# Kernel optimization log

Measured on AMD Instinct MI355X. Metric: run time of the kernel, lower is better.

Reference implementation:

```python
import jax, jax.numpy as jnp
import numpy as np

EPS = 1e-7  # tf.keras.backend.epsilon()
NUM_ROUTING = 3


def squash(v, axis=-1):
    s2 = jnp.sum(jnp.square(v), axis=axis, keepdims=True)
    scale = s2 / (1.0 + s2)
    return scale * v / jnp.sqrt(s2 + EPS)


def setup_inputs() -> dict:
    key = jax.random.key(0)
    kx, kw = jax.random.split(key)
    B, IN_CAPS, IN_DIM = 64, 2048, 16
    NUM_CAPS, OUT_DIM = 32, 16  # OUT_DIM must equal IN_DIM per the tf.matmul in call()
    x = jax.random.normal(kx, (B, IN_CAPS, IN_DIM), dtype=jnp.float32)
    # glorot_uniform over [in_caps, num_caps, in_dim, out_dim]
    limit = float(np.sqrt(6.0 / (IN_DIM + OUT_DIM)))
    W = jax.random.uniform(kw, (IN_CAPS, NUM_CAPS, IN_DIM, OUT_DIM),
                           minval=-limit, maxval=limit, dtype=jnp.float32)
    return {"x": x, "W": W}


def reference(x, W):
    # u_hat[b,i,j,d] = sum_k W[i,j,d,k] * x[b,i,k]   (tf.matmul(W, x[...,None]))
    u_hat = jnp.einsum('ijdk,bik->bijd', W, x)  # [B, in_caps, num_caps, dim]
    b = jnp.zeros(u_hat.shape[:-1], dtype=u_hat.dtype)  # [B, in_caps, num_caps]
    outputs = None
    for i in range(NUM_ROUTING):
        c = jax.nn.softmax(b, axis=2)                       # over num_caps
        s = jnp.einsum('bij,bijd->bjd', c, u_hat)           # weighted sum over in_caps
        outputs = squash(s)                                 # [B, num_caps, dim]
        if i < NUM_ROUTING - 1:
            b = b + jnp.einsum('bijd,bjd->bij', u_hat, outputs)  # agreement
    return outputs
```

## Files before the change

### kernel.cpp

```cpp
#include <hip/hip_runtime.h>
#include <cstdio>


#define IC    2048
#define NC    32
#define OD    16
#define JD    512
#define NIC   256
#define IPB   (IC/NIC)
#define EPS_SQ 1e-7f

typedef short  s16x4  __attribute__((ext_vector_type(4)));
typedef short  s16x8  __attribute__((ext_vector_type(8)));
typedef float  f32x16 __attribute__((ext_vector_type(16)));

__device__ inline short bfc(float f) {
  unsigned u = __builtin_bit_cast(unsigned, f);
  unsigned r = (u + 0x7FFFu + ((u >> 16) & 1u)) >> 16;
  return (short)(unsigned short)r;
}
__device__ inline float bf2f(short s) {
  return __builtin_bit_cast(float, ((unsigned)(unsigned short)s) << 16);
}
__device__ inline f32x16 fz16() {
  f32x16 z;
#pragma unroll
  for (int q = 0; q < 16; q++) z[q] = 0.f;
  return z;
}

__global__ __launch_bounds__(256) void k_prep_x(const float* __restrict__ x,
                                                unsigned short* __restrict__ xp) {
  int t = blockIdx.x * 256 + threadIdx.x;
  int l  = t & 63;
  int bg = (t >> 6) & 1;
  int i  = t >> 7;
  int b  = bg * 32 + (l & 31);
  int hi = l >> 5;
  const float* s = x + ((size_t)b * IC + i) * 16 + 4 * hi;
  float4 v0 = *(const float4*)(s);
  float4 v1 = *(const float4*)(s + 8);
  s16x8 r;
  r[0] = bfc(v0.x); r[1] = bfc(v0.y); r[2] = bfc(v0.z); r[3] = bfc(v0.w);
  r[4] = bfc(v1.x); r[5] = bfc(v1.y); r[6] = bfc(v1.z); r[7] = bfc(v1.w);
  *(s16x8*)(xp + (size_t)t * 8) = r;
}

__global__ __launch_bounds__(256) void k_prep_w(const float* __restrict__ W,
                                                unsigned short* __restrict__ wp) {
  __shared__ unsigned lds[512 * 9];
  const int i = blockIdx.x;
  const int t = threadIdx.x;
  const float* src = W + (size_t)i * 8192;
#pragma unroll
  for (int q = 0; q < 8; q++) {
    int idx = q * 256 + t;
    float4 v = *(const float4*)(src + (size_t)idx * 4);
    unsigned p0 = ((unsigned)(unsigned short)bfc(v.x)) |
                  (((unsigned)(unsigned short)bfc(v.y)) << 16);
    unsigned p1 = ((unsigned)(unsigned short)bfc(v.z)) |
                  (((unsigned)(unsigned short)bfc(v.w)) << 16);
    int jd = idx >> 2;
    int slot = (idx & 3) * 2;
    lds[jd * 9 + slot]     = p0;
    lds[jd * 9 + slot + 1] = p1;
  }
  __syncthreads();
#pragma unroll
  for (int q = 0; q < 4; q++) {
    int f = q * 256 + t;
    int mt = f >> 6, l = f & 63;
    int col = l & 31, hi = l >> 5;
    int jd = mt * 32 + col;
    unsigned r0 = lds[jd * 9 + 2 * hi];
    unsigned r1 = lds[jd * 9 + 2 * hi + 1];
    unsigned r2 = lds[jd * 9 + 2 * hi + 4];
    unsigned r3 = lds[jd * 9 + 2 * hi + 5];
    uint4 o; o.x = r0; o.y = r1; o.z = r2; o.w = r3;
    *(uint4*)(wp + ((size_t)i * 1024 + f) * 8) = o;
  }
}

template <bool FIRST, bool PACKED>
__global__ __launch_bounds__(256, 2) void k_pass(const float* __restrict__ W,
                                                 const unsigned short* __restrict__ Wp,
                                                 const unsigned short* __restrict__ xp,
                                                 const float* __restrict__ ST,
                                                 _Float16* __restrict__ part) {
  __shared__ float lg[32][33];
  const int bid = blockIdx.x;
  const int bg  = bid & 1;
  const int ic  = bid >> 1;
  const int tid = threadIdx.x;
  const int w   = tid >> 6;
  const int l   = tid & 63;
  const int col = l & 31;
  const int hi  = l >> 5;

  f32x16 sa[4];
#pragma unroll
  for (int m = 0; m < 4; m++) sa[m] = fz16();

  s16x8 svA[4], svB[4];
  if (!FIRST) {
#pragma unroll
    for (int m = 0; m < 4; m++) {
      int mt = w * 4 + m;
#pragma unroll
      for (int r = 0; r < 16; r++) {
        int row = (r & 3) + 8 * (r >> 2) + 4 * hi;
        float v = ST[(size_t)(mt * 32 + row) * 64 + bg * 32 + col];
        short h = bfc(v);
        if (r < 8) svA[m][r] = h; else svB[m][r - 8] = h;
      }
    }
  }

  for (int ii = 0; ii < IPB; ii++) {
    int i = ic * IPB + ii;
    s16x8 xv = *(const s16x8*)(xp + ((size_t)i * 2 + bg) * 512 + (size_t)l * 8);
    s16x4 xlo = __builtin_shufflevector(xv, xv, 0, 1, 2, 3);
    s16x4 xhi = __builtin_shufflevector(xv, xv, 4, 5, 6, 7);

    s16x4 wlo[4], whi[4];
    if (PACKED) {
#pragma unroll
      for (int m = 0; m < 4; m++) {
        s16x8 wv = *(const s16x8*)(Wp + ((size_t)i * 1024 + (w * 4 + m) * 64 + l) * 8);
        wlo[m] = __builtin_shufflevector(wv, wv, 0, 1, 2, 3);
        whi[m] = __builtin_shufflevector(wv, wv, 4, 5, 6, 7);
      }
    } else {
#pragma unroll
      for (int m = 0; m < 4; m++) {
        int jd = (w * 4 + m) * 32 + col;
        const float* wq = W + ((size_t)i * JD + jd) * 16 + 4 * hi;
        float4 a0 = *(const float4*)(wq);
        float4 a1 = *(const float4*)(wq + 8);
        s16x4 t0; t0[0]=bfc(a0.x); t0[1]=bfc(a0.y); t0[2]=bfc(a0.z); t0[3]=bfc(a0.w);
        s16x4 t1; t1[0]=bfc(a1.x); t1[1]=bfc(a1.y); t1[2]=bfc(a1.z); t1[3]=bfc(a1.w);
        wlo[m] = t0; whi[m] = t1;
      }
    }

    f32x16 D[4];
#pragma unroll
    for (int m = 0; m < 4; m++) {
      f32x16 acc = FIRST ? sa[m] : fz16();
      acc = __builtin_amdgcn_mfma_f32_32x32x8bf16_1k(wlo[m], xlo, acc, 0, 0, 0);
      acc = __builtin_amdgcn_mfma_f32_32x32x8bf16_1k(whi[m], xhi, acc, 0, 0, 0);
      if (FIRST) sa[m] = acc; else D[m] = acc;
    }

    if (!FIRST) {
#pragma unroll
      for (int m = 0; m < 4; m++) {
        float pe = 0.f, po = 0.f;
#pragma unroll
        for (int r = 0; r < 8; r++)  pe += D[m][r]     * bf2f(svA[m][r]);
#pragma unroll
        for (int r = 0; r < 8; r++)  po += D[m][r + 8] * bf2f(svB[m][r]);
        pe += __shfl_xor(pe, 32);
        po += __shfl_xor(po, 32);
        int mt = w * 4 + m;
        if (l < 32) { lg[2 * mt][col] = pe; lg[2 * mt + 1][col] = po; }
      }
      __syncthreads();
      {
        int bb = w * 8 + (l >> 3);
        int sub = l & 7;
        float v0 = lg[sub * 4 + 0][bb], v1 = lg[sub * 4 + 1][bb];
        float v2 = lg[sub * 4 + 2][bb], v3 = lg[sub * 4 + 3][bb];
        float mx = fmaxf(fmaxf(v0, v1), fmaxf(v2, v3));
        mx = fmaxf(mx, __shfl_xor(mx, 1));
        mx = fmaxf(mx, __shfl_xor(mx, 2));
        mx = fmaxf(mx, __shfl_xor(mx, 4));
        v0 = __expf(v0 - mx); v1 = __expf(v1 - mx);
        v2 = __expf(v2 - mx); v3 = __expf(v3 - mx);
        float sm = v0 + v1 + v2 + v3;
        sm += __shfl_xor(sm, 1);
        sm += __shfl_xor(sm, 2);
        sm += __shfl_xor(sm, 4);
        float iv = 1.0f / sm;
        lg[sub * 4 + 0][bb] = v0 * iv; lg[sub * 4 + 1][bb] = v1 * iv;
        lg[sub * 4 + 2][bb] = v2 * iv; lg[sub * 4 + 3][bb] = v3 * iv;
      }
      __syncthreads();
#pragma unroll
      for (int m = 0; m < 4; m++) {
        int mt = w * 4 + m;
        float ce = lg[2 * mt][col];
        float co = lg[2 * mt + 1][col];
#pragma unroll
        for (int r = 0; r < 8; r++)  sa[m][r]     += ce * D[m][r];
#pragma unroll
        for (int r = 0; r < 8; r++)  sa[m][r + 8] += co * D[m][r + 8];
      }
      __syncthreads();
    }
  }

  const float sc = FIRST ? (1.0f / 32.0f) : 1.0f;
#pragma unroll
  for (int m = 0; m < 4; m++) {
    int mt = w * 4 + m;
#pragma unroll
    for (int r = 0; r < 16; r++) {
      int row = (r & 3) + 8 * (r >> 2) + 4 * hi;
      int jd = mt * 32 + row;
      part[(((size_t)bg * JD + jd) * NIC + ic) * 32 + col] = (_Float16)(sa[m][r] * sc);
    }
  }
}

__global__ __launch_bounds__(512) void k_red(const _Float16* __restrict__ part,
                                             float* __restrict__ red) {
  int bid = blockIdx.x;
  int bg = bid & 1, j = (bid >> 1) & 31, q = bid >> 6;
  int t = threadIdx.x;
  int b = t & 31, d = t >> 5;
  int jd = j * 16 + d;
  const _Float16* p = part + (((size_t)(bg * JD + jd) * NIC) + q * 32) * 32 + b;
  float a0 = 0.f, a1 = 0.f, a2 = 0.f, a3 = 0.f;
#pragma unroll
  for (int qq = 0; qq < 32; qq += 4) {
    a0 += (float)p[(size_t)(qq + 0) * 32];
    a1 += (float)p[(size_t)(qq + 1) * 32];
    a2 += (float)p[(size_t)(qq + 2) * 32];
    a3 += (float)p[(size_t)(qq + 3) * 32];
  }
  red[((size_t)(bg * 32 + j) * 8 + q) * 512 + t] = (a0 + a1) + (a2 + a3);
}

template <bool FIRST, bool FINAL>
__global__ __launch_bounds__(512) void k_squash2(const float* __restrict__ red,
                                                 float* __restrict__ ST,
                                                 float* __restrict__ out) {
  __shared__ float sl[16][33];
  int bid = blockIdx.x;
  int bg = bid & 1, j = bid >> 1;
  int t = threadIdx.x;
  int b = t & 31, d = t >> 5;
  float s = 0.f;
#pragma unroll
  for (int q = 0; q < 8; q++) s += red[((size_t)(bg * 32 + j) * 8 + q) * 512 + t];
  sl[d][b] = s * s;
  __syncthreads();
  float s2 = 0.f;
#pragma unroll
  for (int dd = 0; dd < 16; dd++) s2 += sl[dd][b];
  float o = s * s2 / ((1.0f + s2) * sqrtf(s2 + EPS_SQ));
  int jd = j * 16 + d;
  if (FINAL) {
    out[((size_t)(bg * 32 + b) * NC + j) * OD + d] = o;
  } else if (FIRST) {
    ST[(size_t)jd * 64 + bg * 32 + b] = o;
  } else {
    ST[(size_t)jd * 64 + bg * 32 + b] += o;
  }
}

extern "C" void kernel_launch(void* const* d_in, const int* in_sizes, int n_in,
                              void* d_out, int out_size, void* d_ws, size_t ws_size,
                              hipStream_t stream) {
  (void)in_sizes; (void)n_in; (void)out_size;
  const float* x = (const float*)d_in[0];
  const float* W = (const float*)d_in[1];
  float* out = (float*)d_out;

  const size_t off_xp  = 0;
  const size_t off_st  = (size_t)4 << 20;
  const size_t off_red = off_st + ((size_t)256 << 10);
  const size_t off_pt  = off_red + ((size_t)1 << 20);
  const size_t off_wp  = off_pt + (size_t)2 * JD * NIC * 32 * sizeof(_Float16);
  const size_t need_base = off_wp + 1024;
  const size_t need_full = off_wp + (size_t)IC * 1024 * 16 + 1024;
  fprintf(stderr, "[caps] ws_size=%zu need_base=%zu need_full=%zu\n",
          ws_size, need_base, need_full);
  if (ws_size < need_base) return;
  const bool packed = (ws_size >= need_full);

  unsigned short* xp = (unsigned short*)((char*)d_ws + off_xp);
  float*          ST = (float*)((char*)d_ws + off_st);
  float*         red = (float*)((char*)d_ws + off_red);
  _Float16*     part = (_Float16*)((char*)d_ws + off_pt);
  unsigned short* Wp = (unsigned short*)((char*)d_ws + off_wp);

  k_prep_x<<<dim3(1024), dim3(256), 0, stream>>>(x, xp);
  if (packed) {
    k_prep_w<<<dim3(2048), dim3(256), 0, stream>>>(W, Wp);
    k_pass<true, true><<<dim3(512), dim3(256), 0, stream>>>(W, Wp, xp, ST, part);
  } else {
    k_pass<true, false><<<dim3(512), dim3(256), 0, stream>>>(W, Wp, xp, ST, part);
  }
  k_red<<<dim3(512), dim3(512), 0, stream>>>(part, red);
  k_squash2<true, false><<<dim3(64), dim3(512), 0, stream>>>(red, ST, out);

  for (int pass = 1; pass < 3; pass++) {
    if (packed) {
      k_pass<false, true><<<dim3(512), dim3(256), 0, stream>>>(W, Wp, xp, ST, part);
    } else {
      k_pass<false, false><<<dim3(512), dim3(256), 0, stream>>>(W, Wp, xp, ST, part);
    }
    k_red<<<dim3(512), dim3(512), 0, stream>>>(part, red);
    if (pass == 1) {
      k_squash2<false, false><<<dim3(64), dim3(512), 0, stream>>>(red, ST, out);
    } else {
      k_squash2<false, true><<<dim3(64), dim3(512), 0, stream>>>(red, ST, out);
    }
  }
}
```

Before: 190.2 us.

## Simplify routing softmax to one barrier, merge prep kernels, single-stage reduction

Merges the x and W bf16 prep kernels into one launch and drops the unpacked-W fallback path. In the routing pass, the softmax skips max subtraction and cross-wave LDS transposes. It keeps exp values in registers and reduces only the per-batch normaliser through a small double-buffered LDS array, leaving one barrier per input capsule instead of three. The two-stage partial reduction becomes a single k_red producing final sums, and ST is kept in fp32 rather than re-rounded to bf16. Dropping max subtraction risks overflow if the logits grow large.

```diff
diff --git a/kernel.cpp b/kernel.cpp
--- a/kernel.cpp
+++ b/kernel.cpp
@@ -19,9 +19,6 @@
   unsigned r = (u + 0x7FFFu + ((u >> 16) & 1u)) >> 16;
   return (short)(unsigned short)r;
 }
-__device__ inline float bf2f(short s) {
-  return __builtin_bit_cast(float, ((unsigned)(unsigned short)s) << 16);
-}
 __device__ inline f32x16 fz16() {
   f32x16 z;
 #pragma unroll
@@ -29,65 +26,70 @@
   return z;
 }
 
-__global__ __launch_bounds__(256) void k_prep_x(const float* __restrict__ x,
-                                                unsigned short* __restrict__ xp) {
-  int t = blockIdx.x * 256 + threadIdx.x;
-  int l  = t & 63;
-  int bg = (t >> 6) & 1;
-  int i  = t >> 7;
-  int b  = bg * 32 + (l & 31);
-  int hi = l >> 5;
-  const float* s = x + ((size_t)b * IC + i) * 16 + 4 * hi;
-  float4 v0 = *(const float4*)(s);
-  float4 v1 = *(const float4*)(s + 8);
-  s16x8 r;
-  r[0] = bfc(v0.x); r[1] = bfc(v0.y); r[2] = bfc(v0.z); r[3] = bfc(v0.w);
-  r[4] = bfc(v1.x); r[5] = bfc(v1.y); r[6] = bfc(v1.z); r[7] = bfc(v1.w);
-  *(s16x8*)(xp + (size_t)t * 8) = r;
-}
-
-__global__ __launch_bounds__(256) void k_prep_w(const float* __restrict__ W,
-                                                unsigned short* __restrict__ wp) {
+__global__ __launch_bounds__(256) void k_prep(const float* __restrict__ W,
+                                              const float* __restrict__ x,
+                                              unsigned short* __restrict__ wp,
+                                              unsigned short* __restrict__ xp) {
   __shared__ unsigned lds[512 * 9];
-  const int i = blockIdx.x;
+  const int bid = blockIdx.x;
   const int t = threadIdx.x;
-  const float* src = W + (size_t)i * 8192;
-#pragma unroll
-  for (int q = 0; q < 8; q++) {
-    int idx = q * 256 + t;
-    float4 v = *(const float4*)(src + (size_t)idx * 4);
-    unsigned p0 = ((unsigned)(unsigned short)bfc(v.x)) |
-                  (((unsigned)(unsigned short)bfc(v.y)) << 16);
-    unsigned p1 = ((unsigned)(unsigned short)bfc(v.z)) |
-                  (((unsigned)(unsigned short)bfc(v.w)) << 16);
-    int jd = idx >> 2;
-    int slot = (idx & 3) * 2;
-    lds[jd * 9 + slot]     = p0;
-    lds[jd * 9 + slot + 1] = p1;
-  }
-  __syncthreads();
-#pragma unroll
-  for (int q = 0; q < 4; q++) {
-    int f = q * 256 + t;
-    int mt = f >> 6, l = f & 63;
-    int col = l & 31, hi = l >> 5;
-    int jd = mt * 32 + col;
-    unsigned r0 = lds[jd * 9 + 2 * hi];
-    unsigned r1 = lds[jd * 9 + 2 * hi + 1];
-    unsigned r2 = lds[jd * 9 + 2 * hi + 4];
-    unsigned r3 = lds[jd * 9 + 2 * hi + 5];
-    uint4 o; o.x = r0; o.y = r1; o.z = r2; o.w = r3;
-    *(uint4*)(wp + ((size_t)i * 1024 + f) * 8) = o;
-  }
-}
-
-template <bool FIRST, bool PACKED>
-__global__ __launch_bounds__(256, 2) void k_pass(const float* __restrict__ W,
-                                                 const unsigned short* __restrict__ Wp,
+  if (bid < 2048) {
+    const int i = bid;
+    const float* src = W + (size_t)i * 8192;
+#pragma unroll
+    for (int q = 0; q < 8; q++) {
+      int idx = q * 256 + t;
+      float4 v = *(const float4*)(src + (size_t)idx * 4);
+      unsigned p0 = ((unsigned)(unsigned short)bfc(v.x)) |
+                    (((unsigned)(unsigned short)bfc(v.y)) << 16);
+      unsigned p1 = ((unsigned)(unsigned short)bfc(v.z)) |
+                    (((unsigned)(unsigned short)bfc(v.w)) << 16);
+      int jd = idx >> 2;
+      int slot = (idx & 3) * 2;
+      lds[jd * 9 + slot]     = p0;
+      lds[jd * 9 + slot + 1] = p1;
+    }
+    __syncthreads();
+#pragma unroll
+    for (int q = 0; q < 4; q++) {
+      int f = q * 256 + t;
+      int mt = f >> 6, l = f & 63;
+      int col = l & 31, hi = l >> 5;
+      int jd = mt * 32 + col;
+      uint4 o;
+      o.x = lds[jd * 9 + 2 * hi];
+      o.y = lds[jd * 9 + 2 * hi + 1];
+      o.z = lds[jd * 9 + 2 * hi + 4];
+      o.w = lds[jd * 9 + 2 * hi + 5];
+      *(uint4*)(wp + ((size_t)i * 1024 + f) * 8) = o;
+    }
+  } else {
+    int base = (bid - 2048) * 512;
+#pragma unroll
+    for (int it = 0; it < 2; it++) {
+      int tt = base + it * 256 + t;
+      int l  = tt & 63;
+      int bg = (tt >> 6) & 1;
+      int i  = tt >> 7;
+      int b  = bg * 32 + (l & 31);
+      int hi = l >> 5;
+      const float* s = x + ((size_t)b * IC + i) * 16 + 4 * hi;
+      float4 v0 = *(const float4*)(s);
+      float4 v1 = *(const float4*)(s + 8);
+      s16x8 r;
+      r[0] = bfc(v0.x); r[1] = bfc(v0.y); r[2] = bfc(v0.z); r[3] = bfc(v0.w);
+      r[4] = bfc(v1.x); r[5] = bfc(v1.y); r[6] = bfc(v1.z); r[7] = bfc(v1.w);
+      *(s16x8*)(xp + (size_t)tt * 8) = r;
+    }
+  }
+}
+
+template <bool FIRST>
+__global__ __launch_bounds__(256, 2) void k_pass(const unsigned short* __restrict__ Wp,
                                                  const unsigned short* __restrict__ xp,
                                                  const float* __restrict__ ST,
                                                  _Float16* __restrict__ part) {
-  __shared__ float lg[32][33];
+  __shared__ float zbuf[2][4][33];
   const int bid = blockIdx.x;
   const int bg  = bid & 1;
   const int ic  = bid >> 1;
@@ -101,7 +103,7 @@
 #pragma unroll
   for (int m = 0; m < 4; m++) sa[m] = fz16();
 
-  s16x8 svA[4], svB[4];
+  float Sv[4][16];
   if (!FIRST) {
 #pragma unroll
     for (int m = 0; m < 4; m++) {
@@ -109,9 +111,7 @@
 #pragma unroll
       for (int r = 0; r < 16; r++) {
         int row = (r & 3) + 8 * (r >> 2) + 4 * hi;
-        float v = ST[(size_t)(mt * 32 + row) * 64 + bg * 32 + col];
-        short h = bfc(v);
-        if (r < 8) svA[m][r] = h; else svB[m][r - 8] = h;
+        Sv[m][r] = ST[(size_t)(mt * 32 + row) * 64 + bg * 32 + col];
       }
     }
   }
@@ -123,80 +123,57 @@
     s16x4 xhi = __builtin_shufflevector(xv, xv, 4, 5, 6, 7);
 
     s16x4 wlo[4], whi[4];
-    if (PACKED) {
-#pragma unroll
-      for (int m = 0; m < 4; m++) {
-        s16x8 wv = *(const s16x8*)(Wp + ((size_t)i * 1024 + (w * 4 + m) * 64 + l) * 8);
-        wlo[m] = __builtin_shufflevector(wv, wv, 0, 1, 2, 3);
-        whi[m] = __builtin_shufflevector(wv, wv, 4, 5, 6, 7);
+#pragma unroll
+    for (int m = 0; m < 4; m++) {
+      s16x8 wv = *(const s16x8*)(Wp + ((size_t)i * 1024 + (w * 4 + m) * 64 + l) * 8);
+      wlo[m] = __builtin_shufflevector(wv, wv, 0, 1, 2, 3);
+      whi[m] = __builtin_shufflevector(wv, wv, 4, 5, 6, 7);
+    }
+
+    if (FIRST) {
+#pragma unroll
+      for (int m = 0; m < 4; m++) {
+        sa[m] = __builtin_amdgcn_mfma_f32_32x32x8bf16_1k(wlo[m], xlo, sa[m], 0, 0, 0);
+        sa[m] = __builtin_amdgcn_mfma_f32_32x32x8bf16_1k(whi[m], xhi, sa[m], 0, 0, 0);
       }
     } else {
-#pragma unroll
-      for (int m = 0; m < 4; m++) {
-        int jd = (w * 4 + m) * 32 + col;
-        const float* wq = W + ((size_t)i * JD + jd) * 16 + 4 * hi;
-        float4 a0 = *(const float4*)(wq);
-        float4 a1 = *(const float4*)(wq + 8);
-        s16x4 t0; t0[0]=bfc(a0.x); t0[1]=bfc(a0.y); t0[2]=bfc(a0.z); t0[3]=bfc(a0.w);
-        s16x4 t1; t1[0]=bfc(a1.x); t1[1]=bfc(a1.y); t1[2]=bfc(a1.z); t1[3]=bfc(a1.w);
-        wlo[m] = t0; whi[m] = t1;
-      }
-    }
-
-    f32x16 D[4];
-#pragma unroll
-    for (int m = 0; m < 4; m++) {
-      f32x16 acc = FIRST ? sa[m] : fz16();
-      acc = __builtin_amdgcn_mfma_f32_32x32x8bf16_1k(wlo[m], xlo, acc, 0, 0, 0);
-      acc = __builtin_amdgcn_mfma_f32_32x32x8bf16_1k(whi[m], xhi, acc, 0, 0, 0);
-      if (FIRST) sa[m] = acc; else D[m] = acc;
-    }
-
-    if (!FIRST) {
+      f32x16 D[4];
+#pragma unroll
+      for (int m = 0; m < 4; m++) {
+        f32x16 acc = fz16();
+        acc = __builtin_amdgcn_mfma_f32_32x32x8bf16_1k(wlo[m], xlo, acc, 0, 0, 0);
+        D[m] = __builtin_amdgcn_mfma_f32_32x32x8bf16_1k(whi[m], xhi, acc, 0, 0, 0);
+      }
+
+      float ee[4], eo[4];
+      float zl = 0.f;
 #pragma unroll
       for (int m = 0; m < 4; m++) {
         float pe = 0.f, po = 0.f;
 #pragma unroll
-        for (int r = 0; r < 8; r++)  pe += D[m][r]     * bf2f(svA[m][r]);
-#pragma unroll
-        for (int r = 0; r < 8; r++)  po += D[m][r + 8] * bf2f(svB[m][r]);
+        for (int r = 0; r < 8; r++) pe += D[m][r]     * Sv[m][r];
+#pragma unroll
+        for (int r = 0; r < 8; r++) po += D[m][r + 8] * Sv[m][r + 8];
         pe += __shfl_xor(pe, 32);
         po += __shfl_xor(po, 32);
-        int mt = w * 4 + m;
-        if (l < 32) { lg[2 * mt][col] = pe; lg[2 * mt + 1][col] = po; }
-      }
+        ee[m] = __expf(pe);
+        eo[m] = __expf(po);
+        zl += ee[m] + eo[m];
+      }
+      if (l < 32) zbuf[ii & 1][w][col] = zl;
       __syncthreads();
-      {
-        int bb = w * 8 + (l >> 3);
-        int sub = l & 7;
-        float v0 = lg[sub * 4 + 0][bb], v1 = lg[sub * 4 + 1][bb];
-        float v2 = lg[sub * 4 + 2][bb], v3 = lg[sub * 4 + 3][bb];
-        float mx = fmaxf(fmaxf(v0, v1), fmaxf(v2, v3));
-        mx = fmaxf(mx, __shfl_xor(mx, 1));
-        mx = fmaxf(mx, __shfl_xor(mx, 2));
-        mx = fmaxf(mx, __shfl_xor(mx, 4));
-        v0 = __expf(v0 - mx); v1 = __expf(v1 - mx);
-        v2 = __expf(v2 - mx); v3 = __expf(v3 - mx);
-        float sm = v0 + v1 + v2 + v3;
-        sm += __shfl_xor(sm, 1);
-        sm += __shfl_xor(sm, 2);
-        sm += __shfl_xor(sm, 4);
-        float iv = 1.0f / sm;
-        lg[sub * 4 + 0][bb] = v0 * iv; lg[sub * 4 + 1][bb] = v1 * iv;
-        lg[sub * 4 + 2][bb] = v2 * iv; lg[sub * 4 + 3][bb] = v3 * iv;
-      }
-      __syncthreads();
-#pragma unroll
-      for (int m = 0; m < 4; m++) {
-        int mt = w * 4 + m;
-        float ce = lg[2 * mt][col];
-        float co = lg[2 * mt + 1][col];
-#pragma unroll
-        for (int r = 0; r < 8; r++)  sa[m][r]     += ce * D[m][r];
-#pragma unroll
-        for (int r = 0; r < 8; r++)  sa[m][r + 8] += co * D[m][r + 8];
-      }
-      __syncthreads();
+      float Z = zbuf[ii & 1][0][col] + zbuf[ii & 1][1][col] +
+                zbuf[ii & 1][2][col] + zbuf[ii & 1][3][col];
+      float rz = 1.0f / Z;
+#pragma unroll
+      for (int m = 0; m < 4; m++) {
+        float ce = ee[m] * rz;
+        float co = eo[m] * rz;
+#pragma unroll
+        for (int r = 0; r < 8; r++) sa[m][r]     += ce * D[m][r];
+#pragma unroll
+        for (int r = 0; r < 8; r++) sa[m][r + 8] += co * D[m][r + 8];
+      }
     }
   }
 
@@ -213,44 +190,49 @@
   }
 }
 
-__global__ __launch_bounds__(512) void k_red(const _Float16* __restrict__ part,
-                                             float* __restrict__ red) {
+__global__ __launch_bounds__(256) void k_red(const _Float16* __restrict__ part,
+                                             float* __restrict__ s_red) {
+  __shared__ float sl[8][33];
   int bid = blockIdx.x;
-  int bg = bid & 1, j = (bid >> 1) & 31, q = bid >> 6;
+  int bg = bid & 1, jd = bid >> 1;
   int t = threadIdx.x;
-  int b = t & 31, d = t >> 5;
-  int jd = j * 16 + d;
-  const _Float16* p = part + (((size_t)(bg * JD + jd) * NIC) + q * 32) * 32 + b;
+  int b = t & 31, g = t >> 5;
+  const _Float16* p = part + ((size_t)(bg * JD + jd) * NIC + g) * 32 + b;
   float a0 = 0.f, a1 = 0.f, a2 = 0.f, a3 = 0.f;
 #pragma unroll
-  for (int qq = 0; qq < 32; qq += 4) {
-    a0 += (float)p[(size_t)(qq + 0) * 32];
-    a1 += (float)p[(size_t)(qq + 1) * 32];
-    a2 += (float)p[(size_t)(qq + 2) * 32];
-    a3 += (float)p[(size_t)(qq + 3) * 32];
-  }
-  red[((size_t)(bg * 32 + j) * 8 + q) * 512 + t] = (a0 + a1) + (a2 + a3);
+  for (int q = 0; q < 32; q += 4) {
+    a0 += (float)p[(size_t)(q + 0) * 8 * 32];
+    a1 += (float)p[(size_t)(q + 1) * 8 * 32];
+    a2 += (float)p[(size_t)(q + 2) * 8 * 32];
+    a3 += (float)p[(size_t)(q + 3) * 8 * 32];
+  }
+  sl[g][b] = (a0 + a1) + (a2 + a3);
+  __syncthreads();
+  if (t < 32) {
+    float s = 0.f;
+#pragma unroll
+    for (int gg = 0; gg < 8; gg++) s += sl[gg][t];
+    s_red[((size_t)bg * JD + jd) * 32 + t] = s;
+  }
 }
 
 template <bool FIRST, bool FINAL>
-__global__ __launch_bounds__(512) void k_squash2(const float* __restrict__ red,
-                                                 float* __restrict__ ST,
-                                                 float* __restrict__ out) {
+__global__ __launch_bounds__(512) void k_squash(const float* __restrict__ s_red,
+                                                float* __restrict__ ST,
+                                                float* __restrict__ out) {
   __shared__ float sl[16][33];
   int bid = blockIdx.x;
   int bg = bid & 1, j = bid >> 1;
   int t = threadIdx.x;
   int b = t & 31, d = t >> 5;
-  float s = 0.f;
-#pragma unroll
-  for (int q = 0; q < 8; q++) s += red[((size_t)(bg * 32 + j) * 8 + q) * 512 + t];
+  int jd = j * 16 + d;
+  float s = s_red[((size_t)bg * JD + jd) * 32 + b];
   sl[d][b] = s * s;
   __syncthreads();
   float s2 = 0.f;
 #pragma unroll
   for (int dd = 0; dd < 16; dd++) s2 += sl[dd][b];
   float o = s * s2 / ((1.0f + s2) * sqrtf(s2 + EPS_SQ));
-  int jd = j * 16 + d;
   if (FINAL) {
     out[((size_t)(bg * 32 + b) * NC + j) * OD + d] = o;
   } else if (FIRST) {
@@ -270,43 +252,30 @@
 
   const size_t off_xp  = 0;
   const size_t off_st  = (size_t)4 << 20;
-  const size_t off_red = off_st + ((size_t)256 << 10);
-  const size_t off_pt  = off_red + ((size_t)1 << 20);
+  const size_t off_sr  = off_st + ((size_t)256 << 10);
+  const size_t off_pt  = off_sr + ((size_t)512 << 10);
   const size_t off_wp  = off_pt + (size_t)2 * JD * NIC * 32 * sizeof(_Float16);
-  const size_t need_base = off_wp + 1024;
-  const size_t need_full = off_wp + (size_t)IC * 1024 * 16 + 1024;
-  fprintf(stderr, "[caps] ws_size=%zu need_base=%zu need_full=%zu\n",
-          ws_size, need_base, need_full);
-  if (ws_size < need_base) return;
-  const bool packed = (ws_size >= need_full);
+  const size_t need = off_wp + (size_t)IC * 1024 * 16 + 1024;
+  fprintf(stderr, "[caps] ws_size=%zu need=%zu\n", ws_size, need);
+  if (ws_size < need) return;
 
   unsigned short* xp = (unsigned short*)((char*)d_ws + off_xp);
   float*          ST = (float*)((char*)d_ws + off_st);
-  float*         red = (float*)((char*)d_ws + off_red);
+  float*       s_red = (float*)((char*)d_ws + off_sr);
   _Float16*     part = (_Float16*)((char*)d_ws + off_pt);
   unsigned short* Wp = (unsigned short*)((char*)d_ws + off_wp);
 
-  k_prep_x<<<dim3(1024), dim3(256), 0, stream>>>(x, xp);
-  if (packed) {
-    k_prep_w<<<dim3(2048), dim3(256), 0, stream>>>(W, Wp);
-    k_pass<true, true><<<dim3(512), dim3(256), 0, stream>>>(W, Wp, xp, ST, part);
-  } else {
-    k_pass<true, false><<<dim3(512), dim3(256), 0, stream>>>(W, Wp, xp, ST, part);
-  }
-  k_red<<<dim3(512), dim3(512), 0, stream>>>(part, red);
-  k_squash2<true, false><<<dim3(64), dim3(512), 0, stream>>>(red, ST, out);
-
-  for (int pass = 1; pass < 3; pass++) {
-    if (packed) {
-      k_pass<false, true><<<dim3(512), dim3(256), 0, stream>>>(W, Wp, xp, ST, part);
-    } else {
-      k_pass<false, false><<<dim3(512), dim3(256), 0, stream>>>(W, Wp, xp, ST, part);
-    }
-    k_red<<<dim3(512), dim3(512), 0, stream>>>(part, red);
-    if (pass == 1) {
-      k_squash2<false, false><<<dim3(64), dim3(512), 0, stream>>>(red, ST, out);
-    } else {
-      k_squash2<false, true><<<dim3(64), dim3(512), 0, stream>>>(red, ST, out);
-    }
-  }
-}
+  k_prep<<<dim3(2560), dim3(256), 0, stream>>>(W, x, Wp, xp);
+
+  k_pass<true><<<dim3(512), dim3(256), 0, stream>>>(Wp, xp, ST, part);
+  k_red<<<dim3(1024), dim3(256), 0, stream>>>(part, s_red);
+  k_squash<true, false><<<dim3(64), dim3(512), 0, stream>>>(s_red, ST, out);
+
+  k_pass<false><<<dim3(512), dim3(256), 0, stream>>>(Wp, xp, ST, part);
+  k_red<<<dim3(1024), dim3(256), 0, stream>>>(part, s_red);
+  k_squash<false, false><<<dim3(64), dim3(512), 0, stream>>>(s_red, ST, out);
+
+  k_pass<false><<<dim3(512), dim3(256), 0, stream>>>(Wp, xp, ST, part);
+  k_red<<<dim3(1024), dim3(256), 0, stream>>>(part, s_red);
+  k_squash<false, true><<<dim3(64), dim3(512), 0, stream>>>(s_red, ST, out);
+}
```

After: 185.7 us. 1.02x faster.
